# Kernel optimization log

Measured on AMD Instinct MI355X. Metric: run time of the kernel, lower is better.

The kernel has to match this reference:

```python
import jax, jax.numpy as jnp
import numpy as np

DIM = 1024
HEADS = 16
HEAD_DIM = DIM // HEADS
NEG = -1e30
EPS = 1e-5


def _linear(x, w, b):
    # torch nn.Linear: y = x @ W^T + b, W: [out, in]
    return jnp.einsum('bnd,od->bno', x, w) + b


def _mha(x, ctx, wq, bq, wk, bk, wv, bv, wo, bo, mask):
    B, N, D = x.shape
    M = ctx.shape[1]
    q = _linear(x, wq, bq).reshape(B, N, HEADS, HEAD_DIM).transpose(0, 2, 1, 3)
    k = _linear(ctx, wk, bk).reshape(B, M, HEADS, HEAD_DIM).transpose(0, 2, 1, 3)
    v = _linear(ctx, wv, bv).reshape(B, M, HEADS, HEAD_DIM).transpose(0, 2, 1, 3)
    scores = jnp.einsum('bhqd,bhkd->bhqk', q, k) / np.sqrt(HEAD_DIM).astype(np.float32)
    if mask is not None:
        scores = jnp.where(mask == 0, NEG, scores)
    attn = jax.nn.softmax(scores, axis=-1)  # dropout = identity (eval mode)
    out = jnp.einsum('bhqk,bhkd->bhqd', attn, v)
    out = out.transpose(0, 2, 1, 3).reshape(B, N, D)
    return _linear(out, wo, bo)


def _ln(x, g, b):
    mu = jnp.mean(x, axis=-1, keepdims=True)
    var = jnp.mean(jnp.square(x - mu), axis=-1, keepdims=True)
    return (x - mu) * jax.lax.rsqrt(var + EPS) * g + b


def setup_inputs() -> dict:
    key = jax.random.key(0)
    ks = jax.random.split(key, 24)
    B, N, M = 2, 2048, 1024
    s = 0.02
    d = {
        'x': jax.random.normal(ks[0], (B, N, DIM), jnp.float32),
        'memory': jax.random.normal(ks[1], (B, M, DIM), jnp.float32),
        'mask': jnp.tril(jnp.ones((N, N), jnp.int32))[None, None],
    }
    i = 2
    for p in ['sa', 'ca']:
        for nm in ['q', 'k', 'v', 'o']:
            d[f'{p}_w{nm}'] = jax.random.normal(ks[i], (DIM, DIM), jnp.float32) * s; i += 1
            d[f'{p}_b{nm}'] = jnp.zeros((DIM,), jnp.float32)
    d['ff_w1'] = jax.random.normal(ks[i], (4 * DIM, DIM), jnp.float32) * s; i += 1
    d['ff_b1'] = jnp.zeros((4 * DIM,), jnp.float32)
    d['ff_w2'] = jax.random.normal(ks[i], (DIM, 4 * DIM), jnp.float32) * s; i += 1
    d['ff_b2'] = jnp.zeros((DIM,), jnp.float32)
    for j in (1, 2, 3):
        d[f'ln{j}_g'] = jnp.ones((DIM,), jnp.float32)
        d[f'ln{j}_b'] = jnp.zeros((DIM,), jnp.float32)
    return d


def reference(x, memory, mask,
              sa_wq, sa_bq, sa_wk, sa_bk, sa_wv, sa_bv, sa_wo, sa_bo,
              ca_wq, ca_bq, ca_wk, ca_bk, ca_wv, ca_bv, ca_wo, ca_bo,
              ff_w1, ff_b1, ff_w2, ff_b2,
              ln1_g, ln1_b, ln2_g, ln2_b, ln3_g, ln3_b):
    x = _ln(x + _mha(x, x, sa_wq, sa_bq, sa_wk, sa_bk, sa_wv, sa_bv, sa_wo, sa_bo, mask), ln1_g, ln1_b)
    x = _ln(x + _mha(x, memory, ca_wq, ca_bq, ca_wk, ca_bk, ca_wv, ca_bv, ca_wo, ca_bo, None), ln2_g, ln2_b)
    h = jax.nn.relu(_linear(x, ff_w1, ff_b1))  # dropout = identity (eval)
    x = _ln(x + _linear(h, ff_w2, ff_b2), ln3_g, ln3_b)
    return x
```

## Files before the change

### kernel.cpp

```cpp
#include <hip/hip_runtime.h>


typedef __attribute__((ext_vector_type(8))) short bf16x8;
typedef __attribute__((ext_vector_type(4))) float f32x4;
typedef __attribute__((ext_vector_type(16))) float f32x16;

__device__ __forceinline__ unsigned short f2bf(float f) {
    union { float f; unsigned int u; } v; v.f = f;
    unsigned int r = v.u + 0x7fffu + ((v.u >> 16) & 1u);
    return (unsigned short)(r >> 16);
}
__device__ __forceinline__ float bf2f(unsigned short u) {
    union { unsigned int u; float f; } v; v.u = (unsigned int)u << 16;
    return v.f;
}
__device__ __forceinline__ unsigned int fbits(float f) {
    union { float f; unsigned int u; } v; v.f = f;
    return v.u;
}

struct ConvArgs {
    const float* src[12];
    unsigned short* dst[12];
    int blk_ofs[13];
    int n4[12];
    const float* bq; const float* bk; const float* bv;
    const float* ck; const float* cv;
    float* bqkv; float* bkvc;
};
__global__ __launch_bounds__(256) void conv_multi(ConvArgs a)
{
    int bid = blockIdx.x;
    if (bid >= a.blk_ofs[12]) {
        int i = (bid - a.blk_ofs[12]) * 256 + threadIdx.x;
        if (i < 1024)       a.bqkv[i] = a.bq[i];
        else if (i < 2048)  a.bqkv[i] = a.bk[i - 1024];
        else if (i < 3072)  a.bqkv[i] = a.bv[i - 2048];
        else if (i < 4096)  a.bkvc[i - 3072] = a.ck[i - 3072];
        else if (i < 5120)  a.bkvc[i - 3072] = a.cv[i - 4096];
        return;
    }
    int s = 0;
#pragma unroll
    for (int t = 0; t < 12; ++t) if (bid >= a.blk_ofs[t + 1]) s = t + 1;
    int i = (bid - a.blk_ofs[s]) * 256 + threadIdx.x;
    if (i >= a.n4[s]) return;
    float4 v = ((const float4*)a.src[s])[i];
    ushort4 o;
    o.x = f2bf(v.x); o.y = f2bf(v.y); o.z = f2bf(v.z); o.w = f2bf(v.w);
    ((ushort4*)a.dst[s])[i] = o;
}

template<int TM, int TN, int EPI, int SK>
__device__ __forceinline__ void gemm_body(
    unsigned short (*As)[64], unsigned short (*Bs)[64],
    const unsigned short* __restrict__ A, const unsigned short* __restrict__ W,
    const float* __restrict__ bias, unsigned short* __restrict__ out,
    int K, int Ncols, long slice_stride, int bid, int gx, int zslice)
{
    constexpr int AI = TM / 32;
    constexpr int BJ = TN / 32;

    const int tid  = threadIdx.x;
    const int lane = tid & 63;
    const int wave = tid >> 6;
    const int qd   = lane >> 4;
    const int l15  = lane & 15;
    const int wm   = (wave >> 1) * (TM / 2);
    const int wn   = (wave & 1) * (TN / 2);

    const int gpg = 8 * gx;
    const long m0 = (long)((bid / gpg) * 8 + (bid & 7)) * TM;
    const long n0 = (long)((bid % gpg) >> 3) * TN;

    f32x4 acc[AI][BJ] = {};

    const int srow = lane >> 3;
    const int scol = (((lane & 7) ^ srow)) * 8;
    const unsigned short* Ag = A + (m0 + wave * (8 * AI) + srow) * (long)K + scol;
    const unsigned short* Wg = W + (n0 + wave * (8 * BJ) + srow) * (long)K + scol;

    const int ksl   = K / SK;
    const int kbase = (SK > 1) ? zslice * ksl : 0;

    for (int k0 = kbase; k0 < kbase + ksl; k0 += 64) {
#pragma unroll
        for (int c = 0; c < AI; ++c)
            __builtin_amdgcn_global_load_lds(
                (const __attribute__((address_space(1))) unsigned int*)(Ag + (long)c * 8 * K + k0),
                (__attribute__((address_space(3))) unsigned int*)((char*)&As[0][0] + (wave * AI + c) * 1024),
                16, 0, 0);
#pragma unroll
        for (int c = 0; c < BJ; ++c)
            __builtin_amdgcn_global_load_lds(
                (const __attribute__((address_space(1))) unsigned int*)(Wg + (long)c * 8 * K + k0),
                (__attribute__((address_space(3))) unsigned int*)((char*)&Bs[0][0] + (wave * BJ + c) * 1024),
                16, 0, 0);
        __syncthreads();
#pragma unroll
        for (int kk = 0; kk < 64; kk += 32) {
            const int pg = ((((kk >> 3) + qd)) ^ (l15 & 7)) * 8;
            bf16x8 af[AI], bw[BJ];
#pragma unroll
            for (int i = 0; i < AI; ++i)
                af[i] = *(const bf16x8*)&As[wm + i * 16 + l15][pg];
#pragma unroll
            for (int j = 0; j < BJ; ++j)
                bw[j] = *(const bf16x8*)&Bs[wn + j * 16 + l15][pg];
#pragma unroll
            for (int i = 0; i < AI; ++i)
#pragma unroll
                for (int j = 0; j < BJ; ++j)
                    acc[i][j] = __builtin_amdgcn_mfma_f32_16x16x32_bf16(
                        af[i], bw[j], acc[i][j], 0, 0, 0);
        }
        __syncthreads();
    }

    unsigned short* op = out + ((SK > 1) ? (long)zslice * slice_stride : 0);
#pragma unroll
    for (int j = 0; j < BJ; ++j) {
        long col = n0 + wn + j * 16 + l15;
        float bv = (SK == 1 || zslice == 0) ? bias[col] : 0.f;
#pragma unroll
        for (int i = 0; i < AI; ++i) {
#pragma unroll
            for (int r = 0; r < 4; ++r) {
                long row = m0 + wm + i * 16 + qd * 4 + r;
                float v = acc[i][j][r] + bv;
                if (EPI == 1) v = (v > 0.f) ? v : 0.f;
                op[row * Ncols + col] = f2bf(v);
            }
        }
    }
}

template<int TM, int TN, int EPI, int SK>
__global__ __launch_bounds__(256) void gemm_bt(
    const unsigned short* __restrict__ A, const unsigned short* __restrict__ W,
    const float* __restrict__ bias, unsigned short* __restrict__ out,
    int K, int Ncols, long slice_stride)
{
    __shared__ unsigned short As[TM][64];
    __shared__ unsigned short Bs[TN][64];
    const int bid = blockIdx.y * gridDim.x + blockIdx.x;
    gemm_body<TM, TN, EPI, SK>(As, Bs, A, W, bias, out, K, Ncols, slice_stride,
                               bid, gridDim.x, (int)blockIdx.z);
}

template<int EPI, int SK>
__device__ __forceinline__ void gemm8_body(
    unsigned short* Ab, unsigned short* Bb,
    const unsigned short* __restrict__ A, const unsigned short* __restrict__ W,
    const float* __restrict__ bias, unsigned short* __restrict__ out,
    int K, int Ncols, long slice_stride, int mb, int nb, int zslice)
{
    const int tid  = threadIdx.x;
    const int lane = tid & 63;
    const int wave = tid >> 6;
    const int l31  = lane & 31;
    const int hk   = lane >> 5;
    const int l7   = lane & 7;
    const int wm   = (wave >> 2) * 128;
    const int wn   = (wave & 3) * 64;

    const long m0 = (long)mb * 256;
    const long n0 = (long)nb * 256;

    const int ksl   = K / SK;
    const int kbase = (SK > 1) ? zslice * ksl : 0;
    const int NG    = ksl / 64;

    f32x16 acc[4][2] = {};

    const int srow = tid >> 3;
    const int sgrp = ((tid & 7) ^ (srow & 7)) * 8;
    const unsigned short* Ag = A + (m0 + srow) * (long)K + kbase + sgrp;
    const unsigned short* Wg = W + (n0 + srow) * (long)K + kbase + sgrp;

    auto stA = [&](int db, int r0, int kt) {
        __builtin_amdgcn_global_load_lds(
            (const __attribute__((address_space(1))) unsigned int*)(Ag + (long)r0 * K + kt * 64),
            (__attribute__((address_space(3))) unsigned int*)(Ab + db * 16384 + r0 * 64 + wave * 512),
            16, 0, 0);
    };
    auto stB = [&](int db, int r0, int kt) {
        __builtin_amdgcn_global_load_lds(
            (const __attribute__((address_space(1))) unsigned int*)(Wg + (long)r0 * K + kt * 64),
            (__attribute__((address_space(3))) unsigned int*)(Bb + db * 16384 + r0 * 64 + wave * 512),
            16, 0, 0);
    };
    auto rdA = [&](int db, int row, int kk) -> bf16x8 {
        const int p = (((kk << 1) + hk) ^ l7) << 3;
        return *(const bf16x8*)(Ab + db * 16384 + row * 64 + p);
    };
    auto rdB = [&](int db, int row, int kk) -> bf16x8 {
        const int p = (((kk << 1) + hk) ^ l7) << 3;
        return *(const bf16x8*)(Bb + db * 16384 + row * 64 + p);
    };

#pragma unroll
    for (int h = 0; h < 4; ++h) stA(0, h * 64, 0);
#pragma unroll
    for (int h = 0; h < 4; ++h) stB(0, h * 64, 0);
    if (NG > 1) {
#pragma unroll
        for (int h = 0; h < 4; ++h) stB(1, h * 64, 1);
        stA(1, 0, 1); stA(1, 128, 1);
        asm volatile("s_waitcnt vmcnt(6)" ::: "memory");
    } else {
        asm volatile("s_waitcnt vmcnt(0)" ::: "memory");
    }
    __builtin_amdgcn_s_barrier();

    for (int g = 0; g < NG; ++g) {
        const int db = g & 1, ob = db ^ 1;
        bf16x8 af[2][4], bw[2][4];

        if (g + 1 < NG) { stA(ob, 64, g + 1); stA(ob, 192, g + 1); }

#pragma unroll
        for (int i = 0; i < 2; ++i)
#pragma unroll
            for (int kk = 0; kk < 4; ++kk)
                af[i][kk] = rdA(db, wm + i * 32 + l31, kk);
#pragma unroll
        for (int j = 0; j < 2; ++j)
#pragma unroll
            for (int kk = 0; kk < 4; ++kk)
                bw[j][kk] = rdB(db, wn + j * 32 + l31, kk);
        __builtin_amdgcn_s_setprio(1);
#pragma unroll
        for (int i = 0; i < 2; ++i)
#pragma unroll
            for (int j = 0; j < 2; ++j)
#pragma unroll
                for (int kk = 0; kk < 4; ++kk)
                    acc[i][j] = __builtin_amdgcn_mfma_f32_32x32x16_bf16(
                        af[i][kk], bw[j][kk], acc[i][j], 0, 0, 0);
        __builtin_amdgcn_s_setprio(0);
        __builtin_amdgcn_s_barrier();

        if (g + 2 < NG) {
#pragma unroll
            for (int h = 0; h < 4; ++h) stB(db, h * 64, g + 2);
            stA(db, 0, g + 2); stA(db, 128, g + 2);
        }

#pragma unroll
        for (int i = 0; i < 2; ++i)
#pragma unroll
            for (int kk = 0; kk < 4; ++kk)
                af[i][kk] = rdA(db, wm + 64 + i * 32 + l31, kk);
        __builtin_amdgcn_s_setprio(1);
#pragma unroll
        for (int i = 0; i < 2; ++i)
#pragma unroll
            for (int j = 0; j < 2; ++j)
#pragma unroll
                for (int kk = 0; kk < 4; ++kk)
                    acc[2 + i][j] = __builtin_amdgcn_mfma_f32_32x32x16_bf16(
                        af[i][kk], bw[j][kk], acc[2 + i][j], 0, 0, 0);
        __builtin_amdgcn_s_setprio(0);

        if (g + 2 < NG)      { asm volatile("s_waitcnt vmcnt(6)" ::: "memory"); }
        else if (g + 1 < NG) { asm volatile("s_waitcnt vmcnt(0)" ::: "memory"); }
        __builtin_amdgcn_s_barrier();
    }

    unsigned short* op = out + ((SK > 1) ? (long)zslice * slice_stride : 0);
#pragma unroll
    for (int j = 0; j < 2; ++j) {
        long col = n0 + wn + j * 32 + l31;
        float bv = (SK == 1 || zslice == 0) ? bias[col] : 0.f;
#pragma unroll
        for (int i = 0; i < 4; ++i) {
#pragma unroll
            for (int r = 0; r < 16; ++r) {
                long row = m0 + wm + i * 32 + (r & 3) + 8 * (r >> 2) + 4 * hk;
                float v = acc[i][j][r] + bv;
                if (EPI == 1) v = (v > 0.f) ? v : 0.f;
                op[row * Ncols + col] = f2bf(v);
            }
        }
    }
}

template<int EPI, int SK, int MODE>
__global__ __launch_bounds__(512) void gemm8_bt(
    const unsigned short* __restrict__ A, const unsigned short* __restrict__ W,
    const float* __restrict__ bias, unsigned short* __restrict__ out,
    int K, int Ncols, long slice_stride)
{
    extern __shared__ unsigned short smem[];
    const int bid = blockIdx.x;
    const int x = bid & 7;
    const int s = bid >> 3;
    int mb, nb, z = 0;
    if (MODE == 1) {
        mb = (x >> 1) * 4 + (s & 3);
        nb = (x & 1) * 8 + (s >> 2);
    } else {
        z  = x >> 1;
        mb = (x & 1) * 8 + (s & 7);
        nb = s >> 3;
    }
    gemm8_body<EPI, SK>(smem, smem + 32768, A, W, bias, out, K, Ncols,
                        slice_stride, mb, nb, z);
}

__global__ __launch_bounds__(512) void gemm8_dual(
    const unsigned short* A0, const unsigned short* W0, const float* b0,
    unsigned short* o0, int K0, int N0,
    const unsigned short* A1, const unsigned short* W1, const float* b1,
    unsigned short* o1, int K1, int N1)
{
    extern __shared__ unsigned short smem[];
    const int bid = blockIdx.x;
    const int x = bid & 7;
    const int s = bid >> 3;
    if (s < 24) {
        const int mb = (x >> 1) * 4 + (s & 3);
        const int nb = (x & 1) * 6 + (s >> 2);
        gemm8_body<0, 1>(smem, smem + 32768, A0, W0, b0, o0, K0, N0, 0, mb, nb, 0);
    } else {
        const int t = s - 24;
        const int mb = (x >> 1) * 2 + (t & 1);
        const int nb = (x & 1) * 4 + (t >> 1);
        gemm8_body<0, 1>(smem, smem + 32768, A1, W1, b1, o1, K1, N1, 0, mb, nb, 0);
    }
}

__global__ __launch_bounds__(512) void attn_kernel(
    const unsigned short* __restrict__ Qb, int q_stride,
    const unsigned short* __restrict__ KVb, int kv_stride, int koff, int voff,
    unsigned short* __restrict__ O,
    int Nq, int Mk, int causal)
{
    __shared__ unsigned short Ks[2][64][64];
    __shared__ unsigned short Vs[2][64][64];
    __shared__ unsigned short Ps[8][16][64];

    const int tid  = threadIdx.x;
    const int lane = tid & 63;
    const int wave = tid >> 6;
    const int qd   = lane >> 4;
    const int l15  = lane & 15;
    const int l7   = l15 & 7;
    const int h    = blockIdx.y;
    const int b    = blockIdx.z;
    int jq = blockIdx.x;
    if (causal && (b & 1)) jq = gridDim.x - 1 - jq;
    const int q0 = jq * 128;
    const int tb = q0 + wave * 16;

    const float SCL = 0.125f * 1.44269504f;

    bf16x8 aq0, aq1;
    {
        const unsigned short* qp =
            Qb + (long)(b * Nq + tb + l15) * q_stride + h * 64 + qd * 8;
        aq0 = *(const bf16x8*)qp;
        aq1 = *(const bf16x8*)(qp + 32);
#pragma unroll
        for (int j = 0; j < 8; ++j) {
            aq0[j] = (short)f2bf(bf2f((unsigned short)aq0[j]) * SCL);
            aq1[j] = (short)f2bf(bf2f((unsigned short)aq1[j]) * SCL);
        }
    }

    float lpart[4] = {};
    f32x4 oacc[4] = {};

    const bool vrole = (tid < 256);
    const int vt   = tid & 255;
    const int vj   = vt & 31;
    const int va_k = (vj & 15) + ((vj & 16) << 1);
    const int vfg  = (vt >> 5) * 8;
    const int vpc  = (va_k & 15) * 4 + (va_k >> 4);
    const int krow  = vt >> 3;
    const int kcol  = (vt & 7) * 8;
    const int kcolS = (((vt & 7) ^ (krow & 7))) * 8;

    const unsigned short* Kg = KVb + (long)b * Mk * kv_stride + koff + h * 64;
    const unsigned short* Vg = KVb + (long)b * Mk * kv_stride + voff + h * 64;

    bf16x8 r0, r1;
    auto prefetch = [&](int k0) {
        if (vrole) {
            const unsigned short* v0 = Vg + (long)(k0 + va_k) * kv_stride + vfg;
            r0 = *(const bf16x8*)v0;
            r1 = *(const bf16x8*)(v0 + 16 * kv_stride);
        } else {
            r0 = *(const bf16x8*)(Kg + (long)(k0 + krow) * kv_stride + kcol);
            r1 = *(const bf16x8*)(Kg + (long)(k0 + krow + 32) * kv_stride + kcol);
        }
    };
    auto writeKV = [&](int bs) {
        if (vrole) {
            const unsigned int* pa = (const unsigned int*)&r0;
            const unsigned int* pb = (const unsigned int*)&r1;
#pragma unroll
            for (int w2 = 0; w2 < 4; ++w2) {
                unsigned int d0 = __builtin_amdgcn_perm(pb[w2], pa[w2], 0x05040100u);
                unsigned int d1 = __builtin_amdgcn_perm(pb[w2], pa[w2], 0x07060302u);
                const int rr0 = vfg + 2 * w2, rr1 = rr0 + 1;
                *(unsigned int*)&Vs[bs][rr0][vpc ^ ((rr0 & 7) << 3)] = d0;
                *(unsigned int*)&Vs[bs][rr1][vpc ^ ((rr1 & 7) << 3)] = d1;
            }
        } else {
            *(bf16x8*)&Ks[bs][krow][kcolS]      = r0;
            *(bf16x8*)&Ks[bs][krow + 32][kcolS] = r1;
        }
    };

    const int nk = causal ? (q0 + 128) : Mk;
    const int nt = nk >> 6;

    prefetch(0);
    writeKV(0);
    if (nt > 1) prefetch(64);
    __syncthreads();

    int cur = 0;
    for (int t = 0; t < nt; ++t) {
        const int k0 = t << 6;
        if (t + 1 < nt) {
            writeKV(cur ^ 1);
            if (t + 2 < nt) prefetch((t + 2) << 6);
        }

        if (!causal || (k0 <= tb + 15)) {
            bf16x8 bk[4][2];
#pragma unroll
            for (int kt = 0; kt < 4; ++kt)
#pragma unroll
                for (int c = 0; c < 2; ++c)
                    bk[kt][c] = *(const bf16x8*)&Ks[cur][kt * 16 + l15][((c * 4 + qd) ^ l7) * 8];
            f32x4 s[4];
#pragma unroll
            for (int kt = 0; kt < 4; ++kt) {
                f32x4 z = {};
                z = __builtin_amdgcn_mfma_f32_16x16x32_bf16(aq0, bk[kt][0], z, 0, 0, 0);
                z = __builtin_amdgcn_mfma_f32_16x16x32_bf16(aq1, bk[kt][1], z, 0, 0, 0);
                s[kt] = z;
            }
            const bool needmask = causal && (k0 + 63 > tb);
#pragma unroll
            for (int r = 0; r < 4; ++r) {
                const int qg = tb + qd * 4 + r;
                float e[4];
#pragma unroll
                for (int kt = 0; kt < 4; ++kt) {
                    float ev = __builtin_amdgcn_exp2f(s[kt][r]);
                    if (needmask && (k0 + kt * 16 + l15 > qg)) ev = 0.f;
                    e[kt] = ev;
                }
                lpart[r] += (e[0] + e[1]) + (e[2] + e[3]);
                unsigned int lo = __builtin_amdgcn_perm(fbits(e[1]), fbits(e[0]), 0x07060302u);
                unsigned int hi = __builtin_amdgcn_perm(fbits(e[3]), fbits(e[2]), 0x07060302u);
                uint2 pk; pk.x = lo; pk.y = hi;
                const int prow = qd * 4 + r;
                *(uint2*)&Ps[wave][prow][(l15 * 4) ^ ((prow & 7) << 3)] = pk;
            }
            bf16x8 bv[4][2];
#pragma unroll
            for (int dt = 0; dt < 4; ++dt)
#pragma unroll
                for (int c = 0; c < 2; ++c)
                    bv[dt][c] = *(const bf16x8*)&Vs[cur][dt * 16 + l15][((c * 4 + qd) ^ l7) * 8];
            bf16x8 ap0 = *(const bf16x8*)&Ps[wave][l15][(qd ^ l7) * 8];
            bf16x8 ap1 = *(const bf16x8*)&Ps[wave][l15][((4 + qd) ^ l7) * 8];
#pragma unroll
            for (int dt = 0; dt < 4; ++dt) {
                oacc[dt] = __builtin_amdgcn_mfma_f32_16x16x32_bf16(
                    ap0, bv[dt][0], oacc[dt], 0, 0, 0);
                oacc[dt] = __builtin_amdgcn_mfma_f32_16x16x32_bf16(
                    ap1, bv[dt][1], oacc[dt], 0, 0, 0);
            }
        }
        __syncthreads();
        cur ^= 1;
    }

#pragma unroll
    for (int r = 0; r < 4; ++r) {
        float l = lpart[r];
        l += __shfl_xor(l, 1);
        l += __shfl_xor(l, 2);
        l += __shfl_xor(l, 4);
        l += __shfl_xor(l, 8);
        float inv = 1.f / l;
        long row = (long)(b * Nq + tb + qd * 4 + r);
#pragma unroll
        for (int dt = 0; dt < 4; ++dt)
            O[row * 1024 + h * 64 + dt * 16 + l15] = f2bf(oacc[dt][r] * inv);
    }
}

template<int ND, int RESBF>
__global__ __launch_bounds__(256) void ln_res_kernel(
    const void* __restrict__ res, const unsigned short* __restrict__ delta,
    long dstride, const float* __restrict__ g, const float* __restrict__ beta,
    float* __restrict__ yout, unsigned short* __restrict__ ybf)
{
    __shared__ float red[8];
    const int row = blockIdx.x;
    const int tid = threadIdx.x;
    const long base = (long)row * 1024 + tid * 4;
    float v0, v1, v2, v3;
    if (RESBF) {
        ushort4 a = *(const ushort4*)((const unsigned short*)res + base);
        v0 = bf2f(a.x); v1 = bf2f(a.y); v2 = bf2f(a.z); v3 = bf2f(a.w);
    } else {
        float4 a = *(const float4*)((const float*)res + base);
        v0 = a.x; v1 = a.y; v2 = a.z; v3 = a.w;
    }
#pragma unroll
    for (int t = 0; t < ND; ++t) {
        ushort4 d = *(const ushort4*)(delta + t * dstride + base);
        v0 += bf2f(d.x); v1 += bf2f(d.y); v2 += bf2f(d.z); v3 += bf2f(d.w);
    }
    float s  = v0 + v1 + v2 + v3;
    float ss = v0 * v0 + v1 * v1 + v2 * v2 + v3 * v3;
#pragma unroll
    for (int off = 1; off < 64; off <<= 1) {
        s  += __shfl_xor(s, off);
        ss += __shfl_xor(ss, off);
    }
    const int wave = tid >> 6;
    if ((tid & 63) == 0) { red[wave] = s; red[4 + wave] = ss; }
    __syncthreads();
    float st  = red[0] + red[1] + red[2] + red[3];
    float sst = red[4] + red[5] + red[6] + red[7];
    float mean = st * (1.f / 1024.f);
    float var  = sst * (1.f / 1024.f) - mean * mean;
    float inv  = rsqrtf(var + 1e-5f);
    const int c = tid * 4;
    float y0 = (v0 - mean) * inv * g[c + 0] + beta[c + 0];
    float y1 = (v1 - mean) * inv * g[c + 1] + beta[c + 1];
    float y2 = (v2 - mean) * inv * g[c + 2] + beta[c + 2];
    float y3 = (v3 - mean) * inv * g[c + 3] + beta[c + 3];
    if (yout) *(float4*)(yout + base) = make_float4(y0, y1, y2, y3);
    if (ybf) {
        ushort4 o;
        o.x = f2bf(y0); o.y = f2bf(y1); o.z = f2bf(y2); o.w = f2bf(y3);
        *(ushort4*)(ybf + base) = o;
    }
}

extern "C" void kernel_launch(void* const* d_in, const int* in_sizes, int n_in,
                              void* d_out, int out_size, void* d_ws, size_t ws_size,
                              hipStream_t stream)
{
    const int B = 2, N = 2048, M = 1024, D = 1024, FF = 4096;
    const int TN = B * N;
    const int TM = B * M;
    const size_t MB = 1024 * 1024;

    const float* x     = (const float*)d_in[0];
    const float* mem   = (const float*)d_in[1];
    const float* sa_wq = (const float*)d_in[3];  const float* sa_bq = (const float*)d_in[4];
    const float* sa_wk = (const float*)d_in[5];  const float* sa_bk = (const float*)d_in[6];
    const float* sa_wv = (const float*)d_in[7];  const float* sa_bv = (const float*)d_in[8];
    const float* sa_wo = (const float*)d_in[9];  const float* sa_bo = (const float*)d_in[10];
    const float* ca_wq = (const float*)d_in[11]; const float* ca_bq = (const float*)d_in[12];
    const float* ca_wk = (const float*)d_in[13]; const float* ca_bk = (const float*)d_in[14];
    const float* ca_wv = (const float*)d_in[15]; const float* ca_bv = (const float*)d_in[16];
    const float* ca_wo = (const float*)d_in[17]; const float* ca_bo = (const float*)d_in[18];
    const float* ff_w1 = (const float*)d_in[19]; const float* ff_b1 = (const float*)d_in[20];
    const float* ff_w2 = (const float*)d_in[21]; const float* ff_b2 = (const float*)d_in[22];
    const float* ln1_g = (const float*)d_in[23]; const float* ln1_b = (const float*)d_in[24];
    const float* ln2_g = (const float*)d_in[25]; const float* ln2_b = (const float*)d_in[26];
    const float* ln3_g = (const float*)d_in[27]; const float* ln3_b = (const float*)d_in[28];

    char* w = (char*)d_ws;
    size_t off = 0;
    auto alloc = [&](size_t bytes) -> char* {
        char* p = w + off; off += (bytes + 255) & ~(size_t)255; return p;
    };

    unsigned short* xb   = (unsigned short*)alloc((size_t)TN * D * 2);
    unsigned short* memb = (unsigned short*)alloc((size_t)TM * D * 2);
    unsigned short* wqkv = (unsigned short*)alloc((size_t)3 * D * D * 2);
    unsigned short* wos  = (unsigned short*)alloc((size_t)D * D * 2);
    unsigned short* wqc  = (unsigned short*)alloc((size_t)D * D * 2);
    unsigned short* wkvc = (unsigned short*)alloc((size_t)2 * D * D * 2);
    unsigned short* woc  = (unsigned short*)alloc((size_t)D * D * 2);
    unsigned short* w1b  = (unsigned short*)alloc((size_t)FF * D * 2);
    unsigned short* w2b  = (unsigned short*)alloc((size_t)D * FF * 2);
    char* big = alloc((size_t)80 * MB);
    unsigned short* qkv   = (unsigned short*)big;
    unsigned short* ab    = (unsigned short*)(big + 24 * MB);
    unsigned short* kvb   = (unsigned short*)(big + 32 * MB);
    unsigned short* qb    = (unsigned short*)(big + 40 * MB);
    unsigned short* hb    = (unsigned short*)big;
    unsigned short* tmpbf = (unsigned short*)(big + 48 * MB);
    const long      TSL   = (long)TN * D;
    float* bqkv = (float*)alloc((size_t)3 * D * 4);
    float* bkvc = (float*)alloc((size_t)2 * D * 4);

    ConvArgs ca;
    const float* srcs[12] = {x, mem, sa_wq, sa_wk, sa_wv, sa_wo,
                             ca_wq, ca_wk, ca_wv, ca_wo, ff_w1, ff_w2};
    unsigned short* dsts[12] = {xb, memb, wqkv, wqkv + (size_t)D * D,
                                wqkv + (size_t)2 * D * D, wos, wqc, wkvc,
                                wkvc + (size_t)D * D, woc, w1b, w2b};
    long ns[12] = {(long)TN * D, (long)TM * D, (long)D * D, (long)D * D,
                   (long)D * D, (long)D * D, (long)D * D, (long)D * D,
                   (long)D * D, (long)D * D, (long)FF * D, (long)D * FF};
    int total_blk = 0;
    for (int i = 0; i < 12; ++i) {
        ca.src[i] = srcs[i]; ca.dst[i] = dsts[i];
        ca.n4[i] = (int)(ns[i] / 4);
        ca.blk_ofs[i] = total_blk;
        total_blk += (ca.n4[i] + 255) / 256;
    }
    ca.blk_ofs[12] = total_blk;
    ca.bq = sa_bq; ca.bk = sa_bk; ca.bv = sa_bv; ca.ck = ca_bk; ca.cv = ca_bv;
    ca.bqkv = bqkv; ca.bkvc = bkvc;
    conv_multi<<<dim3(total_blk + 20), dim3(256), 0, stream>>>(ca);

    dim3 blk(256);
    dim3 blk8(512);
    const unsigned int LDS8 = 131072;

    gemm8_dual<<<dim3(256), blk8, LDS8, stream>>>(
        xb,   wqkv, bqkv, qkv, D, 3 * D,
        memb, wkvc, bkvc, kvb, D, 2 * D);

    attn_kernel<<<dim3(N / 128, 16, B), blk8, 0, stream>>>(
        qkv, 3 * D, qkv, 3 * D, D, 2 * D, ab, N, N, 1);
    gemm_bt<128, 64, 0, 2><<<dim3(D / 64, TN / 128, 2), blk, 0, stream>>>(
        ab, wos, sa_bo, tmpbf, D, D, TSL);
    ln_res_kernel<2, 0><<<dim3(TN), blk, 0, stream>>>(
        x, tmpbf, TSL, ln1_g, ln1_b, nullptr, xb);

    gemm_bt<128, 64, 0, 1><<<dim3(D / 64, TN / 128), blk, 0, stream>>>(
        xb, wqc, ca_bq, qb, D, D, 0);
    attn_kernel<<<dim3(N / 128, 16, B), blk8, 0, stream>>>(
        qb, D, kvb, 2 * D, 0, D, ab, N, M, 0);
    gemm_bt<128, 64, 0, 2><<<dim3(D / 64, TN / 128, 2), blk, 0, stream>>>(
        ab, woc, ca_bo, tmpbf, D, D, TSL);
    ln_res_kernel<2, 1><<<dim3(TN), blk, 0, stream>>>(
        xb, tmpbf, TSL, ln2_g, ln2_b, nullptr, xb);

    gemm8_bt<1, 1, 1><<<dim3(256), blk8, LDS8, stream>>>(
        xb, w1b, ff_b1, hb, D, FF, 0);
    gemm8_bt<0, 4, 2><<<dim3(256), blk8, LDS8, stream>>>(
        hb, w2b, ff_b2, tmpbf, FF, D, TSL);
    ln_res_kernel<4, 1><<<dim3(TN), blk, 0, stream>>>(
        xb, tmpbf, TSL, ln3_g, ln3_b, (float*)d_out, nullptr);
}
```

Before: 459.4 us.

## Rewrite attention with 32x32 MFMA and register-resident P via permlane swap

Result: no change. 460.1 us (+0.1%).

```diff
diff --git a/kernel.cpp b/kernel.cpp
--- a/kernel.cpp
+++ b/kernel.cpp
@@ -331,86 +331,75 @@
     }
 }
 
-__global__ __launch_bounds__(512) void attn_kernel(
+__global__ __launch_bounds__(256) void attn_kernel(
     const unsigned short* __restrict__ Qb, int q_stride,
     const unsigned short* __restrict__ KVb, int kv_stride, int koff, int voff,
     unsigned short* __restrict__ O,
     int Nq, int Mk, int causal)
 {
     __shared__ unsigned short Ks[2][64][64];
-    __shared__ unsigned short Vs[2][64][64];
-    __shared__ unsigned short Ps[8][16][64];
+    __shared__ unsigned short Vt[2][64][64];
 
     const int tid  = threadIdx.x;
     const int lane = tid & 63;
     const int wave = tid >> 6;
-    const int qd   = lane >> 4;
-    const int l15  = lane & 15;
-    const int l7   = l15 & 7;
+    const int l31  = lane & 31;
+    const int hk   = lane >> 5;
+    const int l7   = lane & 7;
     const int h    = blockIdx.y;
     const int b    = blockIdx.z;
     int jq = blockIdx.x;
     if (causal && (b & 1)) jq = gridDim.x - 1 - jq;
     const int q0 = jq * 128;
-    const int tb = q0 + wave * 16;
+    const int tb = q0 + wave * 32;
 
     const float SCL = 0.125f * 1.44269504f;
 
-    bf16x8 aq0, aq1;
+    bf16x8 qf[4];
     {
         const unsigned short* qp =
-            Qb + (long)(b * Nq + tb + l15) * q_stride + h * 64 + qd * 8;
-        aq0 = *(const bf16x8*)qp;
-        aq1 = *(const bf16x8*)(qp + 32);
-#pragma unroll
-        for (int j = 0; j < 8; ++j) {
-            aq0[j] = (short)f2bf(bf2f((unsigned short)aq0[j]) * SCL);
-            aq1[j] = (short)f2bf(bf2f((unsigned short)aq1[j]) * SCL);
-        }
-    }
-
-    float lpart[4] = {};
-    f32x4 oacc[4] = {};
-
-    const bool vrole = (tid < 256);
-    const int vt   = tid & 255;
-    const int vj   = vt & 31;
-    const int va_k = (vj & 15) + ((vj & 16) << 1);
-    const int vfg  = (vt >> 5) * 8;
-    const int vpc  = (va_k & 15) * 4 + (va_k >> 4);
-    const int krow  = vt >> 3;
-    const int kcol  = (vt & 7) * 8;
-    const int kcolS = (((vt & 7) ^ (krow & 7))) * 8;
+            Qb + (long)(b * Nq + tb + l31) * q_stride + h * 64 + hk * 8;
+#pragma unroll
+        for (int kk = 0; kk < 4; ++kk) {
+            qf[kk] = *(const bf16x8*)(qp + kk * 16);
+#pragma unroll
+            for (int j = 0; j < 8; ++j)
+                qf[kk][j] = (short)f2bf(bf2f((unsigned short)qf[kk][j]) * SCL);
+        }
+    }
+
+    float lpart = 0.f;
+    f32x16 oacc[2] = {};
+
+    const int krow = tid >> 2;
+    const int kg   = (tid & 3) * 2;
+    const int kp   = tid & 31;
+    const int dvg  = (tid >> 5) * 8;
 
     const unsigned short* Kg = KVb + (long)b * Mk * kv_stride + koff + h * 64;
     const unsigned short* Vg = KVb + (long)b * Mk * kv_stride + voff + h * 64;
 
-    bf16x8 r0, r1;
+    bf16x8 kr0, kr1, vr0, vr1;
     auto prefetch = [&](int k0) {
-        if (vrole) {
-            const unsigned short* v0 = Vg + (long)(k0 + va_k) * kv_stride + vfg;
-            r0 = *(const bf16x8*)v0;
-            r1 = *(const bf16x8*)(v0 + 16 * kv_stride);
-        } else {
-            r0 = *(const bf16x8*)(Kg + (long)(k0 + krow) * kv_stride + kcol);
-            r1 = *(const bf16x8*)(Kg + (long)(k0 + krow + 32) * kv_stride + kcol);
-        }
+        const unsigned short* kpn = Kg + (long)(k0 + krow) * kv_stride + kg * 8;
+        kr0 = *(const bf16x8*)kpn;
+        kr1 = *(const bf16x8*)(kpn + 8);
+        const unsigned short* vpn = Vg + (long)(k0 + 2 * kp) * kv_stride + dvg;
+        vr0 = *(const bf16x8*)vpn;
+        vr1 = *(const bf16x8*)(vpn + kv_stride);
     };
     auto writeKV = [&](int bs) {
-        if (vrole) {
-            const unsigned int* pa = (const unsigned int*)&r0;
-            const unsigned int* pb = (const unsigned int*)&r1;
-#pragma unroll
-            for (int w2 = 0; w2 < 4; ++w2) {
-                unsigned int d0 = __builtin_amdgcn_perm(pb[w2], pa[w2], 0x05040100u);
-                unsigned int d1 = __builtin_amdgcn_perm(pb[w2], pa[w2], 0x07060302u);
-                const int rr0 = vfg + 2 * w2, rr1 = rr0 + 1;
-                *(unsigned int*)&Vs[bs][rr0][vpc ^ ((rr0 & 7) << 3)] = d0;
-                *(unsigned int*)&Vs[bs][rr1][vpc ^ ((rr1 & 7) << 3)] = d1;
-            }
-        } else {
-            *(bf16x8*)&Ks[bs][krow][kcolS]      = r0;
-            *(bf16x8*)&Ks[bs][krow + 32][kcolS] = r1;
+        *(bf16x8*)&Ks[bs][krow][(kg ^ (krow & 7)) * 8]       = kr0;
+        *(bf16x8*)&Ks[bs][krow][((kg + 1) ^ (krow & 7)) * 8] = kr1;
+        const unsigned int* pa = (const unsigned int*)&vr0;
+        const unsigned int* pb = (const unsigned int*)&vr1;
+#pragma unroll
+        for (int w = 0; w < 4; ++w) {
+            unsigned int d0 = __builtin_amdgcn_perm(pb[w], pa[w], 0x05040100u);
+            unsigned int d1 = __builtin_amdgcn_perm(pb[w], pa[w], 0x07060302u);
+            const int dv0 = dvg + 2 * w, dv1 = dv0 + 1;
+            *(unsigned int*)&Vt[bs][dv0][(((kp >> 2) ^ (dv0 & 7)) << 3) + ((2 * kp) & 7)] = d0;
+            *(unsigned int*)&Vt[bs][dv1][(((kp >> 2) ^ (dv1 & 7)) << 3) + ((2 * kp) & 7)] = d1;
         }
     };
 
@@ -430,71 +419,71 @@
             if (t + 2 < nt) prefetch((t + 2) << 6);
         }
 
-        if (!causal || (k0 <= tb + 15)) {
-            bf16x8 bk[4][2];
-#pragma unroll
-            for (int kt = 0; kt < 4; ++kt)
-#pragma unroll
-                for (int c = 0; c < 2; ++c)
-                    bk[kt][c] = *(const bf16x8*)&Ks[cur][kt * 16 + l15][((c * 4 + qd) ^ l7) * 8];
-            f32x4 s[4];
-#pragma unroll
-            for (int kt = 0; kt < 4; ++kt) {
-                f32x4 z = {};
-                z = __builtin_amdgcn_mfma_f32_16x16x32_bf16(aq0, bk[kt][0], z, 0, 0, 0);
-                z = __builtin_amdgcn_mfma_f32_16x16x32_bf16(aq1, bk[kt][1], z, 0, 0, 0);
-                s[kt] = z;
+        if (!causal || (k0 <= tb + 31)) {
+            const bool needmask = causal && (k0 + 63 > tb);
+            const int qg = tb + l31;
+            bf16x8 paf[4];
+            float ls = 0.f;
+#pragma unroll
+            for (int kt = 0; kt < 2; ++kt) {
+                f32x16 z = {};
+#pragma unroll
+                for (int kk = 0; kk < 4; ++kk) {
+                    bf16x8 kf = *(const bf16x8*)
+                        &Ks[cur][kt * 32 + l31][((((kk << 1) + hk)) ^ l7) * 8];
+                    z = __builtin_amdgcn_mfma_f32_32x32x16_bf16(kf, qf[kk], z, 0, 0, 0);
+                }
+                float e[16];
+#pragma unroll
+                for (int r = 0; r < 16; ++r) {
+                    float ev = __builtin_amdgcn_exp2f(z[r]);
+                    if (needmask) {
+                        const int key = k0 + kt * 32 + (r & 3) + 8 * (r >> 2) + 4 * hk;
+                        if (key > qg) ev = 0.f;
+                    }
+                    e[r] = ev;
+                    ls += ev;
+                }
+                unsigned int pk[8];
+#pragma unroll
+                for (int i = 0; i < 8; ++i)
+                    pk[i] = __builtin_amdgcn_perm(fbits(e[2 * i + 1]), fbits(e[2 * i]),
+                                                  0x07060302u);
+                asm volatile("v_permlane32_swap_b32 %0, %1" : "+v"(pk[0]), "+v"(pk[2]));
+                asm volatile("v_permlane32_swap_b32 %0, %1" : "+v"(pk[1]), "+v"(pk[3]));
+                asm volatile("v_permlane32_swap_b32 %0, %1" : "+v"(pk[4]), "+v"(pk[6]));
+                asm volatile("v_permlane32_swap_b32 %0, %1" : "+v"(pk[5]), "+v"(pk[7]));
+                union { unsigned int u[4]; bf16x8 v; } fa, fb;
+                fa.u[0] = pk[0]; fa.u[1] = pk[1]; fa.u[2] = pk[2]; fa.u[3] = pk[3];
+                fb.u[0] = pk[4]; fb.u[1] = pk[5]; fb.u[2] = pk[6]; fb.u[3] = pk[7];
+                paf[kt * 2 + 0] = fa.v;
+                paf[kt * 2 + 1] = fb.v;
             }
-            const bool needmask = causal && (k0 + 63 > tb);
-#pragma unroll
-            for (int r = 0; r < 4; ++r) {
-                const int qg = tb + qd * 4 + r;
-                float e[4];
-#pragma unroll
-                for (int kt = 0; kt < 4; ++kt) {
-                    float ev = __builtin_amdgcn_exp2f(s[kt][r]);
-                    if (needmask && (k0 + kt * 16 + l15 > qg)) ev = 0.f;
-                    e[kt] = ev;
+            lpart += ls;
+#pragma unroll
+            for (int j = 0; j < 2; ++j)
+#pragma unroll
+                for (int kk2 = 0; kk2 < 4; ++kk2) {
+                    bf16x8 vf = *(const bf16x8*)
+                        &Vt[cur][j * 32 + l31][((((kk2 << 1) + hk)) ^ l7) * 8];
+                    oacc[j] = __builtin_amdgcn_mfma_f32_32x32x16_bf16(
+                        paf[kk2], vf, oacc[j], 0, 0, 0);
                 }
-                lpart[r] += (e[0] + e[1]) + (e[2] + e[3]);
-                unsigned int lo = __builtin_amdgcn_perm(fbits(e[1]), fbits(e[0]), 0x07060302u);
-                unsigned int hi = __builtin_amdgcn_perm(fbits(e[3]), fbits(e[2]), 0x07060302u);
-                uint2 pk; pk.x = lo; pk.y = hi;
-                const int prow = qd * 4 + r;
-                *(uint2*)&Ps[wave][prow][(l15 * 4) ^ ((prow & 7) << 3)] = pk;
-            }
-            bf16x8 bv[4][2];
-#pragma unroll
-            for (int dt = 0; dt < 4; ++dt)
-#pragma unroll
-                for (int c = 0; c < 2; ++c)
-                    bv[dt][c] = *(const bf16x8*)&Vs[cur][dt * 16 + l15][((c * 4 + qd) ^ l7) * 8];
-            bf16x8 ap0 = *(const bf16x8*)&Ps[wave][l15][(qd ^ l7) * 8];
-            bf16x8 ap1 = *(const bf16x8*)&Ps[wave][l15][((4 + qd) ^ l7) * 8];
-#pragma unroll
-            for (int dt = 0; dt < 4; ++dt) {
-                oacc[dt] = __builtin_amdgcn_mfma_f32_16x16x32_bf16(
-                    ap0, bv[dt][0], oacc[dt], 0, 0, 0);
-                oacc[dt] = __builtin_amdgcn_mfma_f32_16x16x32_bf16(
-                    ap1, bv[dt][1], oacc[dt], 0, 0, 0);
-            }
         }
         __syncthreads();
         cur ^= 1;
     }
 
-#pragma unroll
-    for (int r = 0; r < 4; ++r) {
-        float l = lpart[r];
-        l += __shfl_xor(l, 1);
-        l += __shfl_xor(l, 2);
-        l += __shfl_xor(l, 4);
-        l += __shfl_xor(l, 8);
-        float inv = 1.f / l;
-        long row = (long)(b * Nq + tb + qd * 4 + r);
-#pragma unroll
-        for (int dt = 0; dt < 4; ++dt)
-            O[row * 1024 + h * 64 + dt * 16 + l15] = f2bf(oacc[dt][r] * inv);
+    float tot = lpart + __shfl_xor(lpart, 32);
+    float inv = 1.f / tot;
+#pragma unroll
+    for (int r = 0; r < 16; ++r) {
+        const int qr = (r & 3) + 8 * (r >> 2) + 4 * hk;
+        float iv = __shfl(inv, qr);
+        const long row = (long)(b * Nq + tb + qr);
+#pragma unroll
+        for (int j = 0; j < 2; ++j)
+            O[row * 1024 + h * 64 + j * 32 + l31] = f2bf(oacc[j][r] * iv);
     }
 }
 
@@ -629,7 +618,7 @@
         xb,   wqkv, bqkv, qkv, D, 3 * D,
         memb, wkvc, bkvc, kvb, D, 2 * D);
 
-    attn_kernel<<<dim3(N / 128, 16, B), blk8, 0, stream>>>(
+    attn_kernel<<<dim3(N / 128, 16, B), blk, 0, stream>>>(
         qkv, 3 * D, qkv, 3 * D, D, 2 * D, ab, N, N, 1);
     gemm_bt<128, 64, 0, 2><<<dim3(D / 64, TN / 128, 2), blk, 0, stream>>>(
         ab, wos, sa_bo, tmpbf, D, D, TSL);
@@ -638,7 +627,7 @@
 
     gemm_bt<128, 64, 0, 1><<<dim3(D / 64, TN / 128), blk, 0, stream>>>(
         xb, wqc, ca_bq, qb, D, D, 0);
-    attn_kernel<<<dim3(N / 128, 16, B), blk8, 0, stream>>>(
+    attn_kernel<<<dim3(N / 128, 16, B), blk, 0, stream>>>(
         qb, D, kvb, 2 * D, 0, D, ab, N, M, 0);
     gemm_bt<128, 64, 0, 2><<<dim3(D / 64, TN / 128, 2), blk, 0, stream>>>(
         ab, woc, ca_bo, tmpbf, D, D, TSL);
```
